# Kernel tuning notes

Measured on AMD Instinct MI355X. Metric: run time of the kernel, lower is better.

## Reference

```python
import jax, jax.numpy as jnp
import numpy as np

B, S, H, D = 8, 1024, 8, 64      # batch, seq_len, num_heads, num_hidden
DM = H * D                        # input model dim = 512
DK = 64.0                         # d_k scale
EPS = 1e-3                        # keras GroupNormalization default epsilon


def setup_inputs() -> dict:
    key = jax.random.key(0)
    ks = jax.random.split(key, 12)
    sc = 1.0 / np.sqrt(DM)
    return {
        "query":  jax.random.normal(ks[0], (B, S, DM), jnp.float32),
        "key":    jax.random.normal(ks[1], (B, S, DM), jnp.float32),
        "values": jax.random.normal(ks[2], (B, S, DM), jnp.float32),
        "Wq": jax.random.normal(ks[3], (DM, 3 * H * D), jnp.float32) * sc,
        "bq": jnp.zeros((3 * H * D,), jnp.float32),
        "Wk": jax.random.normal(ks[4], (DM, 2 * H * D), jnp.float32) * sc,
        "bk": jnp.zeros((2 * H * D,), jnp.float32),
        "Wv": jax.random.normal(ks[5], (DM, H * D), jnp.float32) * sc,
        "bv": jnp.zeros((H * D,), jnp.float32),
        "gamma": jnp.ones((D,), jnp.float32),
        "beta": jnp.zeros((D,), jnp.float32),
        "lam": jax.random.uniform(ks[6], (1,), jnp.float32),          # trainable lambda
        "lambda_init": jax.random.uniform(ks[7], (1,), jnp.float32),  # frozen lambda_init
    }


def reference(query, key, values, Wq, bq, Wk, bk, Wv, bv, gamma, beta, lam, lambda_init):
    # projections -> (B, H, S, *)
    q = (query @ Wq + bq).reshape(B, S, H, 3 * D).transpose(0, 2, 1, 3)
    k = (key @ Wk + bk).reshape(B, S, H, 2 * D).transpose(0, 2, 1, 3)
    v = (values @ Wv + bv).reshape(B, S, H, D).transpose(0, 2, 1, 3)

    q1, q2, gate = jnp.split(q, 3, axis=-1)      # each (B,H,S,D)
    k1, k2 = k[..., :D], k[..., D:]

    inv = 1.0 / jnp.sqrt(jnp.float32(DK))
    s1 = jnp.einsum("bhqd,bhkd->bhqk", q1, k1) * inv
    s2 = jnp.einsum("bhqd,bhkd->bhqk", q2, k2) * inv

    # differential attention: dual softmax combined with learned lambda
    attn = jax.nn.softmax(s1, axis=-1) - lam[0] * jax.nn.softmax(s2, axis=-1)
    out = jnp.einsum("bhqk,bhkd->bhqd", attn, v)      # (B,H,S,D)
    out = out.transpose(0, 2, 1, 3)                    # (B,S,H,D)

    # keras GroupNormalization(groups=H, axis=-1) on channels D:
    # reshape channel dim into (groups, D//H), reduce over all non-batch,
    # non-group axes: (S, H, D//H)
    g = out.reshape(B, S, H, H, D // H)
    mean = jnp.mean(g, axis=(1, 2, 4), keepdims=True)
    var = jnp.var(g, axis=(1, 2, 4), keepdims=True)
    g = (g - mean) * jax.lax.rsqrt(var + EPS)
    out = g.reshape(B, S, H, D) * gamma + beta

    out = out * (1.0 - lambda_init[0])
    out = out * jax.nn.sigmoid(gate.transpose(0, 2, 1, 3))
    return out.reshape(B, S, H * D)
```

## Files before the change

### kernel.cpp

```cpp
#include <hip/hip_runtime.h>
#include <cstdint>
#include <cstddef>

#define B_ 8
#define S_ 1024
#define H_ 8
#define D_ 64
#define DM_ 512

typedef __bf16 bf16x8 __attribute__((ext_vector_type(8)));
typedef float floatx4 __attribute__((ext_vector_type(4)));
typedef float floatx16 __attribute__((ext_vector_type(16)));
typedef unsigned short ushort8 __attribute__((ext_vector_type(8)));
typedef unsigned short ushort4v __attribute__((ext_vector_type(4)));

union Frag { ushort8 us; bf16x8 bf; };

#define MFMA16(a, b, c) __builtin_amdgcn_mfma_f32_16x16x32_bf16((a), (b), (c), 0, 0, 0)
#define MFMA32(a, b, c) __builtin_amdgcn_mfma_f32_32x32x16_bf16((a), (b), (c), 0, 0, 0)

__device__ __forceinline__ unsigned short f2bf(float f) {
  unsigned int u = __float_as_uint(f);
  unsigned int r = (u + 0x7fffu + ((u >> 16) & 1u)) >> 16;
  return (unsigned short)r;
}

__device__ __forceinline__ void gload16(const void* g, void* l) {
  __builtin_amdgcn_global_load_lds(
      (const __attribute__((address_space(1))) unsigned int*)g,
      (__attribute__((address_space(3))) unsigned int*)l, 16, 0, 0);
}

__global__ __launch_bounds__(256) void prep_kernel(
    const float* __restrict__ q, const float* __restrict__ k,
    const float* __restrict__ v, unsigned short* __restrict__ abf,
    const float* __restrict__ Wq, const float* __restrict__ Wk,
    const float* __restrict__ Wv, unsigned short* __restrict__ wt,
    float* __restrict__ partial)
{
  __shared__ unsigned short sT[64][72];
  const int tid = threadIdx.x;
  if (blockIdx.x < 12288) {
    size_t i4 = ((size_t)blockIdx.x * 256 + tid) * 4;
    const size_t SEG = (size_t)4 << 20;
    const float* src = (i4 < SEG) ? (q + i4)
                     : (i4 < 2 * SEG) ? (k + (i4 - SEG))
                                      : (v + (i4 - 2 * SEG));
    floatx4 f = *(const floatx4*)src;
    ushort4v o;
    o[0] = f2bf(f[0]); o[1] = f2bf(f[1]); o[2] = f2bf(f[2]); o[3] = f2bf(f[3]);
    *(ushort4v*)(abf + i4) = o;
    return;
  }
  if (blockIdx.x == 12672) {
    if (tid < 128) partial[tid] = 0.f;
    return;
  }
  const int bid = blockIdx.x - 12288;
  const int k0 = (bid & 7) * 64;
  const int n0 = (bid >> 3) * 64;
  const float* src; int ncols, nb;
  if (n0 < 1536)      { src = Wq; ncols = 1536; nb = n0; }
  else if (n0 < 2560) { src = Wk; ncols = 1024; nb = n0 - 1536; }
  else                { src = Wv; ncols = 512;  nb = n0 - 2560; }

  const int kr0 = tid >> 4, nc4 = (tid & 15) * 4;
  #pragma unroll
  for (int i = 0; i < 4; i++) {
    int kr = kr0 + i * 16;
    floatx4 f = *(const floatx4*)(src + (size_t)(k0 + kr) * ncols + nb + nc4);
    sT[nc4 + 0][kr] = f2bf(f[0]);
    sT[nc4 + 1][kr] = f2bf(f[1]);
    sT[nc4 + 2][kr] = f2bf(f[2]);
    sT[nc4 + 3][kr] = f2bf(f[3]);
  }
  __syncthreads();
  const int nr0 = tid >> 3, kc8 = (tid & 7) * 8;
  #pragma unroll
  for (int i = 0; i < 2; i++) {
    int nr = nr0 + i * 32;
    *(ushort8*)(wt + (size_t)(n0 + nr) * 512 + k0 + kc8) = *(const ushort8*)&sT[nr][kc8];
  }
}

__global__ __launch_bounds__(256) void gemm_kernel(
    const unsigned short* __restrict__ abf, const unsigned short* __restrict__ wt,
    const float* __restrict__ bq, const float* __restrict__ bk,
    const float* __restrict__ bv,
    unsigned short* __restrict__ q1, unsigned short* __restrict__ q2,
    float* __restrict__ gate, unsigned short* __restrict__ k1,
    unsigned short* __restrict__ k2, unsigned short* __restrict__ vT)
{
  const int tid  = threadIdx.x;
  const int wave = tid >> 6;
  const int lane = tid & 63;
  const int l16  = lane & 15;
  const int quad = lane >> 4;
  const int mt = blockIdx.x;
  const int nt = blockIdx.y;
  const int wm = wave & 1, wn = wave >> 1;

  const unsigned short* Asrc =
      abf + (nt < 12 ? 0 : nt < 20 ? ((size_t)4 << 20) : ((size_t)8 << 20));

  __shared__ unsigned short sMem[2 * 128 * 64];
  unsigned short* sA = sMem;
  unsigned short* sB = sMem + 128 * 64;

  floatx4 acc[4][4];
  #pragma unroll
  for (int i = 0; i < 4; i++)
    #pragma unroll
    for (int j = 0; j < 4; j++)
      #pragma unroll
      for (int r = 0; r < 4; r++) acc[i][j][r] = 0.0f;

  const int lrow   = lane >> 3;
  const int gchunk = (lane & 7) ^ lrow;
  const int rkey   = l16 & 7;

  for (int kt = 0; kt < 8; kt++) {
    #pragma unroll
    for (int j = 0; j < 4; j++) {
      int r8 = (wave * 4 + j) * 8;
      gload16(Asrc + (size_t)(mt * 128 + r8 + lrow) * 512 + kt * 64 + gchunk * 8,
              &sA[(wave * 4 + j) * 512]);
      gload16(wt + (size_t)(nt * 128 + r8 + lrow) * 512 + kt * 64 + gchunk * 8,
              &sB[(wave * 4 + j) * 512]);
    }
    __syncthreads();
    #pragma unroll
    for (int c = 0; c < 2; c++) {
      Frag af[4], bf[4];
      #pragma unroll
      for (int mi = 0; mi < 4; mi++)
        af[mi].us = *(const ushort8*)&sA[(wm * 64 + mi * 16 + l16) * 64 +
                                         (((c * 4 + quad) ^ rkey) << 3)];
      #pragma unroll
      for (int ni = 0; ni < 4; ni++)
        bf[ni].us = *(const ushort8*)&sB[(wn * 64 + ni * 16 + l16) * 64 +
                                         (((c * 4 + quad) ^ rkey) << 3)];
      #pragma unroll
      for (int mi = 0; mi < 4; mi++)
        #pragma unroll
        for (int ni = 0; ni < 4; ni++)
          acc[mi][ni] = MFMA16(af[mi].bf, bf[ni].bf, acc[mi][ni]);
    }
    __syncthreads();
  }

  const int gm0 = mt * 128 + wm * 64;
  const int bb  = gm0 >> 10;
  const int s0  = gm0 & 1023;
  const int nseg = nt * 2 + wn;
  unsigned short* sC = sMem + wave * 4096;

  int h, sel = 0; bool isV = false;
  const float* bias_arr; int nb0;
  unsigned short* dstb = nullptr;
  if (nseg < 24)      { h = nseg / 3; sel = nseg % 3; bias_arr = bq; nb0 = nseg * 64;
                        dstb = (sel == 0) ? q1 : (sel == 1) ? q2 : nullptr; }
  else if (nseg < 40) { int t = nseg - 24; h = t >> 1; sel = t & 1;
                        bias_arr = bk; nb0 = t * 64; dstb = sel ? k2 : k1; }
  else                { h = nseg - 40; isV = true; bias_arr = bv; nb0 = (nseg - 40) * 64; }

  if (dstb != nullptr || isV) {
    const float scl = (nseg < 24) ? 0.125f : 1.0f;
    #pragma unroll
    for (int ni = 0; ni < 4; ni++) {
      float bv_ = bias_arr[nb0 + ni * 16 + l16];
      #pragma unroll
      for (int mi = 0; mi < 4; mi++)
        #pragma unroll
        for (int r = 0; r < 4; r++) {
          float val = (acc[mi][ni][r] + bv_) * scl;
          int ml = mi * 16 + quad * 4 + r;
          int nl = ni * 16 + l16;
          if (!isV) {
            int ch = (nl >> 3) ^ (ml & 7);
            sC[ml * 64 + (ch << 3) + (nl & 7)] = f2bf(val);
          } else {
            int ch = (ml >> 3) ^ (nl & 7);
            sC[nl * 64 + (ch << 3) + (ml & 7)] = f2bf(val);
          }
        }
    }
    const int rr = lane >> 3, cc = lane & 7;
    if (!isV) {
      unsigned short* base = dstb + ((size_t)(bb * H_ + h) * S_ + s0) * D_;
      #pragma unroll
      for (int j = 0; j < 8; j++) {
        int row = j * 8 + rr;
        int logc = cc ^ (row & 7);
        ushort8 valv = *(const ushort8*)&sC[row * 64 + cc * 8];
        *(ushort8*)(base + (size_t)row * D_ + logc * 8) = valv;
      }
    } else {
      unsigned short* base = vT + ((size_t)(bb * H_ + h) * D_) * S_ + s0;
      #pragma unroll
      for (int j = 0; j < 8; j++) {
        int drow = j * 8 + rr;
        int logc = cc ^ (drow & 7);
        ushort8 valv = *(const ushort8*)&sC[drow * 64 + cc * 8];
        *(ushort8*)(base + (size_t)drow * S_ + logc * 8) = valv;
      }
    }
  } else {
    #pragma unroll
    for (int ni = 0; ni < 4; ni++) {
      float bv_ = bias_arr[nb0 + ni * 16 + l16];
      #pragma unroll
      for (int mi = 0; mi < 4; mi++)
        #pragma unroll
        for (int r = 0; r < 4; r++) {
          int s = s0 + mi * 16 + quad * 4 + r;
          int d = ni * 16 + l16;
          gate[((size_t)(bb * H_ + h) * S_ + s) * D_ + d] = acc[mi][ni][r] + bv_;
        }
    }
  }
}

__global__ __launch_bounds__(256, 4) void attn_kernel(
    const unsigned short* __restrict__ q1, const unsigned short* __restrict__ q2,
    const unsigned short* __restrict__ k1, const unsigned short* __restrict__ k2,
    const unsigned short* __restrict__ vT, const float* __restrict__ lamp,
    float* __restrict__ O, float* __restrict__ partial)
{
  const int tid   = threadIdx.x;
  const int wave  = tid >> 6;
  const int lane  = tid & 63;
  const int l32   = lane & 31;
  const int lhalf = lane >> 5;
  const int kh    = wave & 1;
  const int qh    = wave >> 1;
  const int bh = blockIdx.x & 63;
  const int qt = blockIdx.x >> 6;
  const int q0 = qt * 64;

  __shared__ unsigned short sMem[5 * 4096];
  unsigned short* sK1 = sMem;
  unsigned short* sK2 = sMem + 4096;
  unsigned short* sVt = sMem + 8192;
  unsigned short* sP1 = sMem + 12288;
  unsigned short* sP2 = sMem + 16384;

  const size_t qrowoff = ((size_t)bh * S_ + q0 + qh * 32 + l32) * D_ + lhalf * 8;
  Frag qb1[4], qb2[4];
  #pragma unroll
  for (int ks = 0; ks < 4; ks++) {
    qb1[ks].us = *(const ushort8*)(q1 + qrowoff + ks * 16);
    qb2[ks].us = *(const ushort8*)(q2 + qrowoff + ks * 16);
  }

  floatx16 o1, o2;
  #pragma unroll
  for (int r = 0; r < 16; r++) { o1[r] = 0.f; o2[r] = 0.f; }
  float l1 = 0.f, l2 = 0.f;

  const unsigned short* kb1 = k1 + (size_t)bh * S_ * D_;
  const unsigned short* kb2 = k2 + (size_t)bh * S_ * D_;
  const unsigned short* vb  = vT + (size_t)bh * D_ * S_;

  const int srow = lane >> 3;
  const int sgch = (lane & 7) ^ srow;
  const int akey = l32 & 7;
  const int mrow = kh * 32 + l32;

  for (int kt = 0; kt < 16; kt++) {
    #pragma unroll
    for (int i = 0; i < 2; i++) {
      int r0 = wave * 16 + i * 8;
      gload16(kb1 + (size_t)(kt * 64 + r0 + srow) * 64 + sgch * 8, &sK1[r0 * 64]);
      gload16(kb2 + (size_t)(kt * 64 + r0 + srow) * 64 + sgch * 8, &sK2[r0 * 64]);
      gload16(vb  + (size_t)(r0 + srow) * S_ + kt * 64 + sgch * 8, &sVt[r0 * 64]);
    }
    __syncthreads();

    floatx16 s1, s2;
    #pragma unroll
    for (int r = 0; r < 16; r++) { s1[r] = 0.f; s2[r] = 0.f; }
    #pragma unroll
    for (int ks = 0; ks < 4; ks++) {
      int phys = ((ks * 2 + lhalf) ^ akey) << 3;
      Frag kf1; kf1.us = *(const ushort8*)&sK1[mrow * 64 + phys];
      s1 = MFMA32(kf1.bf, qb1[ks].bf, s1);
      Frag kf2; kf2.us = *(const ushort8*)&sK2[mrow * 64 + phys];
      s2 = MFMA32(kf2.bf, qb2[ks].bf, s2);
    }

    const int qrow = (qh * 32 + l32) * 64;
    #pragma unroll
    for (int p = 0; p < 8; p++) {
      int key = kh * 32 + 2 * (p & 1) + 8 * (p >> 1) + 4 * lhalf;
      int addr = qrow + (((key >> 3) ^ akey) << 3) + (key & 7);
      float a1 = __expf(s1[2 * p]), b1 = __expf(s1[2 * p + 1]);
      l1 += a1 + b1;
      *(uint32_t*)&sP1[addr] = (uint32_t)f2bf(a1) | ((uint32_t)f2bf(b1) << 16);
      float a2 = __expf(s2[2 * p]), b2 = __expf(s2[2 * p + 1]);
      l2 += a2 + b2;
      *(uint32_t*)&sP2[addr] = (uint32_t)f2bf(a2) | ((uint32_t)f2bf(b2) << 16);
    }
    __syncthreads();

    #pragma unroll
    for (int ks = 0; ks < 4; ks++) {
      int phys = ((ks * 2 + lhalf) ^ akey) << 3;
      Frag vf; vf.us = *(const ushort8*)&sVt[mrow * 64 + phys];
      Frag pf1; pf1.us = *(const ushort8*)&sP1[qrow + phys];
      o1 = MFMA32(vf.bf, pf1.bf, o1);
      Frag pf2; pf2.us = *(const ushort8*)&sP2[qrow + phys];
      o2 = MFMA32(vf.bf, pf2.bf, o2);
    }
    __syncthreads();
  }

  l1 += __shfl_xor(l1, 32, 64);
  l2 += __shfl_xor(l2, 32, 64);
  float* sL = (float*)(sMem + 10240);
  float* sG = (float*)(sMem + 10752);
  if (lane < 32) {
    sL[(0 * 2 + kh) * 64 + qh * 32 + l32] = l1;
    sL[(1 * 2 + kh) * 64 + qh * 32 + l32] = l2;
  }
  __syncthreads();

  const int q = qh * 32 + l32;
  float i1 = 1.0f / (sL[q] + sL[64 + q]);
  float i2 = lamp[0] / (sL[128 + q] + sL[192 + q]);
  float* fO = (float*)sMem;
  #pragma unroll
  for (int r = 0; r < 16; r++) {
    int d = kh * 32 + (r & 3) + 8 * (r >> 2) + 4 * lhalf;
    fO[d * 65 + q] = o1[r] * i1 - o2[r] * i2;
  }
  if (tid < 16) sG[tid] = 0.f;
  __syncthreads();

  float ss = 0.f, ss2 = 0.f;
  float* Ob = O + ((size_t)bh * S_ + q0) * D_;
  #pragma unroll
  for (int i = 0; i < 4; i++) {
    int qrw = i * 16 + (tid >> 4);
    int d0 = (tid & 15) * 4;
    floatx4 v;
    #pragma unroll
    for (int j = 0; j < 4; j++) {
      v[j] = fO[(d0 + j) * 65 + qrw];
      ss += v[j]; ss2 += v[j] * v[j];
    }
    *(floatx4*)(Ob + (size_t)qrw * D_ + d0) = v;
  }
  ss  += __shfl_xor(ss, 16, 64);  ss  += __shfl_xor(ss, 32, 64);  ss  += __shfl_xor(ss, 1, 64);
  ss2 += __shfl_xor(ss2, 16, 64); ss2 += __shfl_xor(ss2, 32, 64); ss2 += __shfl_xor(ss2, 1, 64);
  if (lane < 16 && (lane & 1) == 0) {
    int j = lane >> 1;
    atomicAdd(&sG[j * 2],     ss);
    atomicAdd(&sG[j * 2 + 1], ss2);
  }
  __syncthreads();
  if (tid < 16) atomicAdd(&partial[(bh >> 3) * 16 + tid], sG[tid]);
}

__global__ __launch_bounds__(256) void final_kernel(
    const float* __restrict__ O, const float* __restrict__ gate,
    const float* __restrict__ partial, const float* __restrict__ gamma,
    const float* __restrict__ beta, const float* __restrict__ li,
    float* __restrict__ out)
{
  int e = blockIdx.x * 256 + threadIdx.x;
  int d  = e & 63;
  int hh = (e >> 6) & 7;
  int s  = (e >> 9) & 1023;
  int b  = e >> 19;
  size_t oidx = (size_t)(b * 8 + hh) * 65536 + (size_t)s * 64 + d;
  int g = b * 8 + (d >> 3);
  float S1 = partial[g * 2];
  float S2 = partial[g * 2 + 1];
  float mean = S1 * (1.0f / 65536.f);
  float inv  = rsqrtf(S2 * (1.0f / 65536.f) - mean * mean + 0.001f);
  float x = (O[oidx] - mean) * inv;
  x = x * gamma[d] + beta[d];
  x *= (1.0f - li[0]);
  float gt = gate[oidx];
  x *= 1.0f / (1.0f + __expf(-gt));
  out[e] = x;
}

extern "C" void kernel_launch(void* const* d_in, const int* in_sizes, int n_in,
                              void* d_out, int out_size, void* d_ws, size_t ws_size,
                              hipStream_t stream)
{
  const float* query  = (const float*)d_in[0];
  const float* key    = (const float*)d_in[1];
  const float* values = (const float*)d_in[2];
  const float* Wq = (const float*)d_in[3];
  const float* bq = (const float*)d_in[4];
  const float* Wk = (const float*)d_in[5];
  const float* bk = (const float*)d_in[6];
  const float* Wv = (const float*)d_in[7];
  const float* bv = (const float*)d_in[8];
  const float* gamma = (const float*)d_in[9];
  const float* beta  = (const float*)d_in[10];
  const float* lam   = (const float*)d_in[11];
  const float* lami  = (const float*)d_in[12];
  float* out = (float*)d_out;

  char* ws = (char*)d_ws;
  const size_t MB = (size_t)1 << 20;
  unsigned short* abf = (unsigned short*)(ws);
  float*          O   = (float*)(ws);
  unsigned short* wt  = (unsigned short*)(ws + 24 * MB);
  float* partial      = (float*)(ws + 27 * MB);
  unsigned short* q1  = (unsigned short*)(ws + 28 * MB);
  unsigned short* q2  = (unsigned short*)(ws + 36 * MB);
  unsigned short* k1  = (unsigned short*)(ws + 44 * MB);
  unsigned short* k2  = (unsigned short*)(ws + 52 * MB);
  unsigned short* vT  = (unsigned short*)(ws + 60 * MB);
  float* gate         = (float*)(ws + 68 * MB);

  prep_kernel<<<12673, 256, 0, stream>>>(query, key, values, abf, Wq, Wk, Wv, wt,
                                         partial);
  gemm_kernel<<<dim3(64, 24), 256, 0, stream>>>(abf, wt, bq, bk, bv,
                                                q1, q2, gate, k1, k2, vT);
  attn_kernel<<<dim3(1024), 256, 0, stream>>>(q1, q2, k1, k2, vT, lam, O, partial);
  final_kernel<<<16384, 256, 0, stream>>>(O, gate, partial, gamma, beta, lami, out);
}
```

Baseline: 253.4 us.

## Load K and V fragments directly from global into registers, dropping LDS staging

K1, K2 and V^T tiles are now read straight from global memory into MFMA register fragments instead of being staged through LDS with async global_load_lds, which removes one barrier per key tile and shrinks LDS use. The P write uses v_cvt_pk_bf16_f32 with 8-byte stores, and setprio brackets raise priority around the MFMA sections. The cost is duplicated global reads, since each K/V row is now fetched by both qh wave pairs, plus more register pressure and exposed global latency in the loop.

```diff
diff --git a/kernel.cpp b/kernel.cpp
--- a/kernel.cpp
+++ b/kernel.cpp
@@ -13,6 +13,7 @@
 typedef float floatx16 __attribute__((ext_vector_type(16)));
 typedef unsigned short ushort8 __attribute__((ext_vector_type(8)));
 typedef unsigned short ushort4v __attribute__((ext_vector_type(4)));
+typedef unsigned int uint32x2 __attribute__((ext_vector_type(2)));
 
 union Frag { ushort8 us; bf16x8 bf; };
 
@@ -23,6 +24,12 @@
   unsigned int u = __float_as_uint(f);
   unsigned int r = (u + 0x7fffu + ((u >> 16) & 1u)) >> 16;
   return (unsigned short)r;
+}
+
+__device__ __forceinline__ uint32_t cvtpk_bf16(float lo, float hi) {
+  uint32_t r;
+  asm("v_cvt_pk_bf16_f32 %0, %1, %2" : "=v"(r) : "v"(lo), "v"(hi));
+  return r;
 }
 
 __device__ __forceinline__ void gload16(const void* g, void* l) {
@@ -238,12 +245,9 @@
   const int qt = blockIdx.x >> 6;
   const int q0 = qt * 64;
 
-  __shared__ unsigned short sMem[5 * 4096];
-  unsigned short* sK1 = sMem;
-  unsigned short* sK2 = sMem + 4096;
-  unsigned short* sVt = sMem + 8192;
-  unsigned short* sP1 = sMem + 12288;
-  unsigned short* sP2 = sMem + 16384;
+  __shared__ unsigned short sMem[8864];
+  unsigned short* sP1 = sMem;
+  unsigned short* sP2 = sMem + 4096;
 
   const size_t qrowoff = ((size_t)bh * S_ + q0 + qh * 32 + l32) * D_ + lhalf * 8;
   Frag qb1[4], qb2[4];
@@ -258,67 +262,69 @@
   for (int r = 0; r < 16; r++) { o1[r] = 0.f; o2[r] = 0.f; }
   float l1 = 0.f, l2 = 0.f;
 
-  const unsigned short* kb1 = k1 + (size_t)bh * S_ * D_;
-  const unsigned short* kb2 = k2 + (size_t)bh * S_ * D_;
-  const unsigned short* vb  = vT + (size_t)bh * D_ * S_;
-
-  const int srow = lane >> 3;
-  const int sgch = (lane & 7) ^ srow;
   const int akey = l32 & 7;
   const int mrow = kh * 32 + l32;
+  const int qrow = (qh * 32 + l32) * 64;
+
+  const unsigned short* kp1 = k1 + (size_t)bh * S_ * D_ + (size_t)mrow * D_ + lhalf * 8;
+  const unsigned short* kp2 = k2 + (size_t)bh * S_ * D_ + (size_t)mrow * D_ + lhalf * 8;
+  const unsigned short* vp  = vT + (size_t)bh * D_ * S_ + (size_t)mrow * S_ + lhalf * 8;
 
   for (int kt = 0; kt < 16; kt++) {
-    #pragma unroll
-    for (int i = 0; i < 2; i++) {
-      int r0 = wave * 16 + i * 8;
-      gload16(kb1 + (size_t)(kt * 64 + r0 + srow) * 64 + sgch * 8, &sK1[r0 * 64]);
-      gload16(kb2 + (size_t)(kt * 64 + r0 + srow) * 64 + sgch * 8, &sK2[r0 * 64]);
-      gload16(vb  + (size_t)(r0 + srow) * S_ + kt * 64 + sgch * 8, &sVt[r0 * 64]);
+    Frag kf1[4], kf2[4], vf[4];
+    #pragma unroll
+    for (int ks = 0; ks < 4; ks++) {
+      kf1[ks].us = *(const ushort8*)(kp1 + kt * (64 * D_) + ks * 16);
+      kf2[ks].us = *(const ushort8*)(kp2 + kt * (64 * D_) + ks * 16);
+    }
+    #pragma unroll
+    for (int ks = 0; ks < 4; ks++)
+      vf[ks].us = *(const ushort8*)(vp + kt * 64 + ks * 16);
+
+    floatx16 s1, s2;
+    #pragma unroll
+    for (int r = 0; r < 16; r++) { s1[r] = 0.f; s2[r] = 0.f; }
+    __builtin_amdgcn_s_setprio(1);
+    #pragma unroll
+    for (int ks = 0; ks < 4; ks++) {
+      s1 = MFMA32(kf1[ks].bf, qb1[ks].bf, s1);
+      s2 = MFMA32(kf2[ks].bf, qb2[ks].bf, s2);
+    }
+    __builtin_amdgcn_s_setprio(0);
+
+    #pragma unroll
+    for (int qd = 0; qd < 4; qd++) {
+      const int addr = qrow + (((kh * 4 + qd) ^ akey) << 3) + 4 * lhalf;
+      float e0 = __expf(s1[4 * qd + 0]), e1 = __expf(s1[4 * qd + 1]);
+      float e2 = __expf(s1[4 * qd + 2]), e3 = __expf(s1[4 * qd + 3]);
+      l1 += (e0 + e1) + (e2 + e3);
+      uint32x2 w1; w1[0] = cvtpk_bf16(e0, e1); w1[1] = cvtpk_bf16(e2, e3);
+      *(uint32x2*)&sP1[addr] = w1;
+      float f0 = __expf(s2[4 * qd + 0]), f1 = __expf(s2[4 * qd + 1]);
+      float f2 = __expf(s2[4 * qd + 2]), f3 = __expf(s2[4 * qd + 3]);
+      l2 += (f0 + f1) + (f2 + f3);
+      uint32x2 w2; w2[0] = cvtpk_bf16(f0, f1); w2[1] = cvtpk_bf16(f2, f3);
+      *(uint32x2*)&sP2[addr] = w2;
     }
     __syncthreads();
 
-    floatx16 s1, s2;
-    #pragma unroll
-    for (int r = 0; r < 16; r++) { s1[r] = 0.f; s2[r] = 0.f; }
+    __builtin_amdgcn_s_setprio(1);
     #pragma unroll
     for (int ks = 0; ks < 4; ks++) {
       int phys = ((ks * 2 + lhalf) ^ akey) << 3;
-      Frag kf1; kf1.us = *(const ushort8*)&sK1[mrow * 64 + phys];
-      s1 = MFMA32(kf1.bf, qb1[ks].bf, s1);
-      Frag kf2; kf2.us = *(const ushort8*)&sK2[mrow * 64 + phys];
-      s2 = MFMA32(kf2.bf, qb2[ks].bf, s2);
-    }
-
-    const int qrow = (qh * 32 + l32) * 64;
-    #pragma unroll
-    for (int p = 0; p < 8; p++) {
-      int key = kh * 32 + 2 * (p & 1) + 8 * (p >> 1) + 4 * lhalf;
-      int addr = qrow + (((key >> 3) ^ akey) << 3) + (key & 7);
-      float a1 = __expf(s1[2 * p]), b1 = __expf(s1[2 * p + 1]);
-      l1 += a1 + b1;
-      *(uint32_t*)&sP1[addr] = (uint32_t)f2bf(a1) | ((uint32_t)f2bf(b1) << 16);
-      float a2 = __expf(s2[2 * p]), b2 = __expf(s2[2 * p + 1]);
-      l2 += a2 + b2;
-      *(uint32_t*)&sP2[addr] = (uint32_t)f2bf(a2) | ((uint32_t)f2bf(b2) << 16);
-    }
-    __syncthreads();
-
-    #pragma unroll
-    for (int ks = 0; ks < 4; ks++) {
-      int phys = ((ks * 2 + lhalf) ^ akey) << 3;
-      Frag vf; vf.us = *(const ushort8*)&sVt[mrow * 64 + phys];
       Frag pf1; pf1.us = *(const ushort8*)&sP1[qrow + phys];
-      o1 = MFMA32(vf.bf, pf1.bf, o1);
+      o1 = MFMA32(vf[ks].bf, pf1.bf, o1);
       Frag pf2; pf2.us = *(const ushort8*)&sP2[qrow + phys];
-      o2 = MFMA32(vf.bf, pf2.bf, o2);
-    }
+      o2 = MFMA32(vf[ks].bf, pf2.bf, o2);
+    }
+    __builtin_amdgcn_s_setprio(0);
     __syncthreads();
   }
 
   l1 += __shfl_xor(l1, 32, 64);
   l2 += __shfl_xor(l2, 32, 64);
-  float* sL = (float*)(sMem + 10240);
-  float* sG = (float*)(sMem + 10752);
+  float* sL = (float*)(sMem + 8320);
+  float* sG = (float*)(sMem + 8832);
   if (lane < 32) {
     sL[(0 * 2 + kh) * 64 + qh * 32 + l32] = l1;
     sL[(1 * 2 + kh) * 64 + qh * 32 + l32] = l2;
```

Result: slower. 325.7 us (+28.5%).

## Pipeline K/V staging with PV and S phases, use exp2 and packed bf16 convert

Applied to the files above, without the earlier changes.

Restructures the attention key loop so that the next tile's K loads are issued while the current PV MFMAs run, and V loads are issued after PV finishes. Explicit vmcnt/lgkmcnt waits and raw barriers replace __syncthreads. The log2(e) factor is folded into the Q projection scale so softmax can use exp2 directly. P is packed with v_cvt_pk_bf16_f32 and stored as 64-bit writes, and s_setprio is raised around the MFMA blocks. The hand-counted waits are fragile and could race if the load counts do not match.

```diff
diff --git a/kernel.cpp b/kernel.cpp
--- a/kernel.cpp
+++ b/kernel.cpp
@@ -13,6 +13,7 @@
 typedef float floatx16 __attribute__((ext_vector_type(16)));
 typedef unsigned short ushort8 __attribute__((ext_vector_type(8)));
 typedef unsigned short ushort4v __attribute__((ext_vector_type(4)));
+typedef unsigned int uint32x2 __attribute__((ext_vector_type(2)));
 
 union Frag { ushort8 us; bf16x8 bf; };
 
@@ -23,6 +24,12 @@
   unsigned int u = __float_as_uint(f);
   unsigned int r = (u + 0x7fffu + ((u >> 16) & 1u)) >> 16;
   return (unsigned short)r;
+}
+
+__device__ __forceinline__ uint32_t cvtpk_bf16(float lo, float hi) {
+  uint32_t r;
+  asm("v_cvt_pk_bf16_f32 %0, %1, %2" : "=v"(r) : "v"(lo), "v"(hi));
+  return r;
 }
 
 __device__ __forceinline__ void gload16(const void* g, void* l) {
@@ -165,7 +172,7 @@
   else                { h = nseg - 40; isV = true; bias_arr = bv; nb0 = (nseg - 40) * 64; }
 
   if (dstb != nullptr || isV) {
-    const float scl = (nseg < 24) ? 0.125f : 1.0f;
+    const float scl = (nseg < 24) ? 0.125f * 1.44269504088896f : 1.0f;
     #pragma unroll
     for (int ni = 0; ni < 4; ni++) {
       float bv_ = bias_arr[nb0 + ni * 16 + l16];
@@ -266,20 +273,29 @@
   const int sgch = (lane & 7) ^ srow;
   const int akey = l32 & 7;
   const int mrow = kh * 32 + l32;
-
-  for (int kt = 0; kt < 16; kt++) {
+  const int qrow = (qh * 32 + l32) * 64;
+
+  auto STAGE_K = [&](int kt) {
     #pragma unroll
     for (int i = 0; i < 2; i++) {
       int r0 = wave * 16 + i * 8;
       gload16(kb1 + (size_t)(kt * 64 + r0 + srow) * 64 + sgch * 8, &sK1[r0 * 64]);
       gload16(kb2 + (size_t)(kt * 64 + r0 + srow) * 64 + sgch * 8, &sK2[r0 * 64]);
-      gload16(vb  + (size_t)(r0 + srow) * S_ + kt * 64 + sgch * 8, &sVt[r0 * 64]);
-    }
-    __syncthreads();
-
+    }
+  };
+  auto STAGE_V = [&](int kt) {
+    #pragma unroll
+    for (int i = 0; i < 2; i++) {
+      int r0 = wave * 16 + i * 8;
+      gload16(vb + (size_t)(r0 + srow) * S_ + kt * 64 + sgch * 8, &sVt[r0 * 64]);
+    }
+  };
+
+  auto S_PHASE = [&]() {
     floatx16 s1, s2;
     #pragma unroll
     for (int r = 0; r < 16; r++) { s1[r] = 0.f; s2[r] = 0.f; }
+    __builtin_amdgcn_s_setprio(1);
     #pragma unroll
     for (int ks = 0; ks < 4; ks++) {
       int phys = ((ks * 2 + lhalf) ^ akey) << 3;
@@ -288,21 +304,29 @@
       Frag kf2; kf2.us = *(const ushort8*)&sK2[mrow * 64 + phys];
       s2 = MFMA32(kf2.bf, qb2[ks].bf, s2);
     }
-
-    const int qrow = (qh * 32 + l32) * 64;
-    #pragma unroll
-    for (int p = 0; p < 8; p++) {
-      int key = kh * 32 + 2 * (p & 1) + 8 * (p >> 1) + 4 * lhalf;
-      int addr = qrow + (((key >> 3) ^ akey) << 3) + (key & 7);
-      float a1 = __expf(s1[2 * p]), b1 = __expf(s1[2 * p + 1]);
-      l1 += a1 + b1;
-      *(uint32_t*)&sP1[addr] = (uint32_t)f2bf(a1) | ((uint32_t)f2bf(b1) << 16);
-      float a2 = __expf(s2[2 * p]), b2 = __expf(s2[2 * p + 1]);
-      l2 += a2 + b2;
-      *(uint32_t*)&sP2[addr] = (uint32_t)f2bf(a2) | ((uint32_t)f2bf(b2) << 16);
-    }
-    __syncthreads();
-
+    __builtin_amdgcn_s_setprio(0);
+    #pragma unroll
+    for (int qd = 0; qd < 4; qd++) {
+      const int addr = qrow + (((kh * 4 + qd) ^ akey) << 3) + 4 * lhalf;
+      float e0 = __builtin_amdgcn_exp2f(s1[4 * qd + 0]);
+      float e1 = __builtin_amdgcn_exp2f(s1[4 * qd + 1]);
+      float e2 = __builtin_amdgcn_exp2f(s1[4 * qd + 2]);
+      float e3 = __builtin_amdgcn_exp2f(s1[4 * qd + 3]);
+      l1 += (e0 + e1) + (e2 + e3);
+      uint32x2 w1; w1[0] = cvtpk_bf16(e0, e1); w1[1] = cvtpk_bf16(e2, e3);
+      *(uint32x2*)&sP1[addr] = w1;
+      float f0 = __builtin_amdgcn_exp2f(s2[4 * qd + 0]);
+      float f1 = __builtin_amdgcn_exp2f(s2[4 * qd + 1]);
+      float f2 = __builtin_amdgcn_exp2f(s2[4 * qd + 2]);
+      float f3 = __builtin_amdgcn_exp2f(s2[4 * qd + 3]);
+      l2 += (f0 + f1) + (f2 + f3);
+      uint32x2 w2; w2[0] = cvtpk_bf16(f0, f1); w2[1] = cvtpk_bf16(f2, f3);
+      *(uint32x2*)&sP2[addr] = w2;
+    }
+  };
+
+  auto PV_PHASE = [&]() {
+    __builtin_amdgcn_s_setprio(1);
     #pragma unroll
     for (int ks = 0; ks < 4; ks++) {
       int phys = ((ks * 2 + lhalf) ^ akey) << 3;
@@ -312,8 +336,32 @@
       Frag pf2; pf2.us = *(const ushort8*)&sP2[qrow + phys];
       o2 = MFMA32(vf.bf, pf2.bf, o2);
     }
-    __syncthreads();
-  }
+    __builtin_amdgcn_s_setprio(0);
+  };
+
+  STAGE_K(0);
+  STAGE_V(0);
+  asm volatile("s_waitcnt vmcnt(2)" ::: "memory");
+  __builtin_amdgcn_s_barrier();
+  S_PHASE();
+  asm volatile("s_waitcnt vmcnt(0) lgkmcnt(0)" ::: "memory");
+  __builtin_amdgcn_s_barrier();
+
+  for (int kt = 1; kt < 16; kt++) {
+    STAGE_K(kt);
+    PV_PHASE();
+    asm volatile("s_waitcnt lgkmcnt(0)" ::: "memory");
+    __builtin_amdgcn_s_barrier();
+    STAGE_V(kt);
+    asm volatile("s_waitcnt vmcnt(2)" ::: "memory");
+    __builtin_amdgcn_s_barrier();
+    S_PHASE();
+    asm volatile("s_waitcnt vmcnt(0) lgkmcnt(0)" ::: "memory");
+    __builtin_amdgcn_s_barrier();
+  }
+  PV_PHASE();
+  asm volatile("s_waitcnt lgkmcnt(0)" ::: "memory");
+  __builtin_amdgcn_s_barrier();
 
   l1 += __shfl_xor(l1, 32, 64);
   l2 += __shfl_xor(l2, 32, 64);
```

Result: faster. 219.9 us (-13.2%).
